# Kernel optimization log

Hardware: AMD Instinct MI355X
Metric: run time of the kernel (lower is better)

## Reference

```python
import jax, jax.numpy as jnp
import numpy as np

N_NODES = 100_000
N_EDGES = 3_200_000  # avg in-degree 32
N_CLASSES = 16
TEMP = 0.5


def setup_inputs() -> dict:
    key = jax.random.key(0)
    k1, k2, k3 = jax.random.split(key, 3)
    src = jax.random.randint(k1, (N_EDGES,), 0, N_NODES, dtype=jnp.int32)
    # guarantee every node has at least one incoming edge so scatter-mean
    # and the sharpening normalization are well-defined
    dst = jnp.concatenate([
        jnp.arange(N_NODES, dtype=jnp.int32),
        jax.random.randint(k2, (N_EDGES - N_NODES,), 0, N_NODES, dtype=jnp.int32),
    ])
    edge_index = jnp.stack([src, dst], axis=0)  # [2, E]
    # positive predictions (log is taken downstream)
    aug_pred = jax.random.uniform(k3, (N_NODES, N_CLASSES), jnp.float32, 1e-3, 1.0)
    return {"edge_index": edge_index, "aug_pred": aug_pred}


def reference(edge_index, aug_pred):
    src = edge_index[0]  # message source nodes
    dst = edge_index[1]  # aggregation targets
    E = edge_index.shape[1]

    # scatter-mean aggregation: avg_pred[i] = mean_{e: dst[e]=i} aug_pred[src[e]]
    msg = aug_pred[src]                                   # [E, C]
    sums = jax.ops.segment_sum(msg, dst, num_segments=N_NODES)
    cnt = jax.ops.segment_sum(jnp.ones((E,), aug_pred.dtype), dst,
                              num_segments=N_NODES)
    avg_pred = sums / jnp.maximum(cnt, 1.0)[:, None]      # [N, C]

    # temperature sharpening + normalize
    p = avg_pred ** (1.0 / TEMP)
    sharp_avg_pred = p / jnp.sum(p, axis=1, keepdims=True)

    # edge-indexed gathers; dst side is detached in the original
    s = (avg_pred + 1e-10)[src]                            # [E, C]
    d = jax.lax.stop_gradient(sharp_avg_pred + 1e-10)[dst]  # [E, C]

    cr_loss = (d * jnp.log(d) - d * jnp.log(s)).sum(axis=1)  # [E]
    return cr_loss.mean()
```

## Files before the change

kernel.cpp:

```cpp
#include <hip/hip_runtime.h>

#define NCLS 16
#define NB 391
#define BSH 8
#define TILE 4096
#define KPT 16
#define PREB 512
#define BMAX 9216
#define ACAP 9

static __device__ __forceinline__ float bflo(unsigned u) {
  return __uint_as_float(u << 16);
}
static __device__ __forceinline__ float bfhi(unsigned u) {
  return __uint_as_float(u & 0xFFFF0000u);
}
static __device__ __forceinline__ unsigned f2bf1(float f) {
  unsigned u = __float_as_uint(f);
  return (u + 0x7FFF + ((u >> 16) & 1)) >> 16;
}
static __device__ __forceinline__ unsigned packbf(float a, float b) {
  return f2bf1(a) | (f2bf1(b) << 16);
}

__global__ void pre_kernel(const int* __restrict__ dstv, int* __restrict__ bcnt, int E,
                           const float2* __restrict__ aug, unsigned* __restrict__ augh, int n2) {
  __shared__ int lh[NB];
  if (blockIdx.x < PREB) {
    for (int t = threadIdx.x; t < NB; t += 256) lh[t] = 0;
    __syncthreads();
    int stride = PREB * 256;
    for (int i = blockIdx.x * 256 + threadIdx.x; i < E; i += stride)
      atomicAdd(&lh[dstv[i] >> BSH], 1);
    __syncthreads();
    for (int t = threadIdx.x; t < NB; t += 256) {
      int v = lh[t];
      if (v) atomicAdd(&bcnt[t], v);
    }
  } else {
    int i = (blockIdx.x - PREB) * 256 + threadIdx.x;
    if (i < n2) {
      float2 v = aug[i];
      augh[i] = packbf(v.x, v.y);
    }
  }
}

__global__ void bscan_kernel(const int* __restrict__ bcnt, int* __restrict__ bbase,
                             int* __restrict__ gcur) {
  __shared__ int tmp[512];
  int t = threadIdx.x;
  int x = (t < NB) ? bcnt[t] : 0;
  tmp[t] = x;
  __syncthreads();
  for (int o = 1; o < 512; o <<= 1) {
    int v = (t >= o) ? tmp[t - o] : 0;
    __syncthreads();
    tmp[t] += v;
    __syncthreads();
  }
  if (t < NB) { int e = tmp[t] - x; bbase[t] = e; gcur[t] = e; }
  if (t == NB - 1) bbase[NB] = tmp[t];
}

__global__ void __launch_bounds__(256) bin_kernel(const int* __restrict__ srcv,
                                                  const int* __restrict__ dstv,
                                                  int* __restrict__ gcur,
                                                  int* __restrict__ packed, int E) {
  __shared__ int hist[NB];
  __shared__ int off[NB];
  __shared__ int delta[NB];
  __shared__ int part[16];
  __shared__ int2 stag[TILE];
  int tid = threadIdx.x;
  int base = blockIdx.x * TILE;
  int cnt = min(TILE, E - base);
  for (int t = tid; t < NB; t += 256) hist[t] = 0;
  __syncthreads();
  int myw[KPT];
  int myp[KPT];
#pragma unroll
  for (int k = 0; k < KPT; k++) {
    int idx = tid + k * 256;
    myw[k] = -1;
    myp[k] = 0;
    if (idx < cnt) {
      int s = srcv[base + idx], d = dstv[base + idx];
      int b = d >> BSH;
      int r = atomicAdd(&hist[b], 1);
      myw[k] = s | ((d & 255) << 17);
      myp[k] = (b << 12) | r;
    }
  }
  __syncthreads();
  if (tid < 16) {
    int s = 0;
    int lo = tid * 25, hiX = min(NB, lo + 25);
    for (int j = lo; j < hiX; j++) { int v = hist[j]; off[j] = s; s += v; }
    part[tid] = s;
  }
  __syncthreads();
  if (tid == 0) {
    int run = 0;
    for (int j = 0; j < 16; j++) { int v = part[j]; part[j] = run; run += v; }
  }
  __syncthreads();
  for (int t = tid; t < NB; t += 256) off[t] += part[t / 25];
  __syncthreads();
  for (int t = tid; t < NB; t += 256) {
    int c = hist[t];
    int gb = c ? atomicAdd(&gcur[t], c) : 0;
    delta[t] = gb - off[t];
  }
  __syncthreads();
#pragma unroll
  for (int k = 0; k < KPT; k++) {
    if (myw[k] >= 0) {
      int b = myp[k] >> 12, r = myp[k] & 4095;
      int p = off[b] + r;
      int2 w;
      w.x = myw[k];
      w.y = p + delta[b];
      stag[p] = w;
    }
  }
  __syncthreads();
  for (int i = tid; i < cnt; i += 256) {
    int2 w = stag[i];
    packed[w.y] = w.x;
  }
}

__global__ void __launch_bounds__(1024) agg_kernel(const int* __restrict__ bbase,
                                                   const int* __restrict__ packed,
                                                   const unsigned* __restrict__ augh,
                                                   unsigned* __restrict__ logs,
                                                   float* __restrict__ dvec,
                                                   double* __restrict__ acc, int N) {
  __shared__ int ssrc[BMAX];
  __shared__ int hist[256];
  __shared__ int off[256];
  __shared__ float red[16];
  int tid = threadIdx.x;
  int b = blockIdx.x;
  int rbeg = bbase[b], rend = bbase[b + 1];
  if (tid < 256) hist[tid] = 0;
  __syncthreads();
  int myw[ACAP];
  int myr[ACAP];
#pragma unroll
  for (int k = 0; k < ACAP; k++) {
    int i = rbeg + tid + k * 1024;
    int w = (i < rend) ? packed[i] : -1;
    myw[k] = w;
    myr[k] = (w >= 0) ? atomicAdd(&hist[w >> 17], 1) : 0;
  }
  __syncthreads();
  if (tid < 64) {
    int h0 = hist[4 * tid], h1 = hist[4 * tid + 1];
    int h2 = hist[4 * tid + 2], h3 = hist[4 * tid + 3];
    int tot = h0 + h1 + h2 + h3;
    int inc = tot;
#pragma unroll
    for (int o = 1; o < 64; o <<= 1) {
      int u = __shfl_up(inc, o, 64);
      if (tid >= o) inc += u;
    }
    int exc = inc - tot;
    off[4 * tid] = exc;
    off[4 * tid + 1] = exc + h0;
    off[4 * tid + 2] = exc + h0 + h1;
    off[4 * tid + 3] = exc + h0 + h1 + h2;
  }
  __syncthreads();
#pragma unroll
  for (int k = 0; k < ACAP; k++) {
    int w = myw[k];
    if (w >= 0) ssrc[off[w >> 17] + myr[k]] = w & 0x1FFFF;
  }
  __syncthreads();
  int node = tid >> 2, lane = tid & 3;
  int boff = off[node];
  int deg = hist[node];
  double s0 = 0., s1 = 0., s2 = 0., s3 = 0.;
  int wsh = lane << 1;
  int e = 0;
  for (; e + 8 <= deg; e += 8) {
    int q0 = ssrc[boff + e],     q1 = ssrc[boff + e + 1];
    int q2 = ssrc[boff + e + 2], q3 = ssrc[boff + e + 3];
    int q4 = ssrc[boff + e + 4], q5 = ssrc[boff + e + 5];
    int q6 = ssrc[boff + e + 6], q7 = ssrc[boff + e + 7];
    uint2 g0 = *reinterpret_cast<const uint2*>(augh + ((size_t)q0 << 3) + wsh);
    uint2 g1 = *reinterpret_cast<const uint2*>(augh + ((size_t)q1 << 3) + wsh);
    uint2 g2 = *reinterpret_cast<const uint2*>(augh + ((size_t)q2 << 3) + wsh);
    uint2 g3 = *reinterpret_cast<const uint2*>(augh + ((size_t)q3 << 3) + wsh);
    uint2 g4 = *reinterpret_cast<const uint2*>(augh + ((size_t)q4 << 3) + wsh);
    uint2 g5 = *reinterpret_cast<const uint2*>(augh + ((size_t)q5 << 3) + wsh);
    uint2 g6 = *reinterpret_cast<const uint2*>(augh + ((size_t)q6 << 3) + wsh);
    uint2 g7 = *reinterpret_cast<const uint2*>(augh + ((size_t)q7 << 3) + wsh);
    s0 += (double)bflo(g0.x) + (double)bflo(g1.x) + (double)bflo(g2.x) + (double)bflo(g3.x) +
          (double)bflo(g4.x) + (double)bflo(g5.x) + (double)bflo(g6.x) + (double)bflo(g7.x);
    s1 += (double)bfhi(g0.x) + (double)bfhi(g1.x) + (double)bfhi(g2.x) + (double)bfhi(g3.x) +
          (double)bfhi(g4.x) + (double)bfhi(g5.x) + (double)bfhi(g6.x) + (double)bfhi(g7.x);
    s2 += (double)bflo(g0.y) + (double)bflo(g1.y) + (double)bflo(g2.y) + (double)bflo(g3.y) +
          (double)bflo(g4.y) + (double)bflo(g5.y) + (double)bflo(g6.y) + (double)bflo(g7.y);
    s3 += (double)bfhi(g0.y) + (double)bfhi(g1.y) + (double)bfhi(g2.y) + (double)bfhi(g3.y) +
          (double)bfhi(g4.y) + (double)bfhi(g5.y) + (double)bfhi(g6.y) + (double)bfhi(g7.y);
  }
  for (; e < deg; e++) {
    int q0 = ssrc[boff + e];
    uint2 g0 = *reinterpret_cast<const uint2*>(augh + ((size_t)q0 << 3) + wsh);
    s0 += (double)bflo(g0.x); s1 += (double)bfhi(g0.x);
    s2 += (double)bflo(g0.y); s3 += (double)bfhi(g0.y);
  }
  double dinv = 1.0 / (double)(deg > 0 ? deg : 1);
  float a0 = (float)(s0 * dinv), a1 = (float)(s1 * dinv);
  float a2 = (float)(s2 * dinv), a3 = (float)(s3 * dinv);
  float p2 = a0 * a0 + a1 * a1 + a2 * a2 + a3 * a3;
  p2 += __shfl_xor(p2, 1, 64);
  p2 += __shfl_xor(p2, 2, 64);
  float ip = 1.0f / p2;
  float d0 = a0 * a0 * ip + 1e-10f, d1 = a1 * a1 * ip + 1e-10f;
  float d2 = a2 * a2 * ip + 1e-10f, d3 = a3 * a3 * ip + 1e-10f;
  float h = d0 * __logf(d0) + d1 * __logf(d1) + d2 * __logf(d2) + d3 * __logf(d3);
  h += __shfl_xor(h, 1, 64);
  h += __shfl_xor(h, 2, 64);
  int g = (b << BSH) + node;
  float contrib = 0.f;
  if (g < N) {
    uint2 lw;
    lw.x = packbf(__logf(a0 + 1e-10f), __logf(a1 + 1e-10f));
    lw.y = packbf(__logf(a2 + 1e-10f), __logf(a3 + 1e-10f));
    *reinterpret_cast<uint2*>(logs + ((size_t)g << 3) + wsh) = lw;
    float4 dd;
    dd.x = d0; dd.y = d1; dd.z = d2; dd.w = d3;
    *reinterpret_cast<float4*>(dvec + ((size_t)g << 4) + (lane << 2)) = dd;
    if (lane == 0) contrib = (float)deg * h;
  }
#pragma unroll
  for (int o = 32; o >= 1; o >>= 1) contrib += __shfl_xor(contrib, o, 64);
  if ((tid & 63) == 0) red[tid >> 6] = contrib;
  __syncthreads();
  if (tid == 0) {
    float s = 0.f;
#pragma unroll
    for (int wv = 0; wv < 16; wv++) s += red[wv];
    atomicAdd(acc, (double)s);
  }
}

#define ASTR 17
__global__ void __launch_bounds__(1024) loss_kernel(const int* __restrict__ bbase,
                                                    const int* __restrict__ packed,
                                                    const unsigned* __restrict__ logs,
                                                    const float* __restrict__ dvec,
                                                    double* __restrict__ acc, int N) {
  __shared__ float sdv[256 * ASTR];
  __shared__ double red[16];
  int tid = threadIdx.x;
  int b = blockIdx.x;
  int rbeg = bbase[b], rend = bbase[b + 1];
  int nb0 = b << BSH;
  {
    const float4* gsrc = reinterpret_cast<const float4*>(dvec + ((size_t)nb0 << 4));
    int nvalid = min(256, N - nb0);
    int nf4 = nvalid * 4;
    for (int i = tid; i < nf4; i += 1024) {
      float4 v = gsrc[i];
      float* r = sdv + (i >> 2) * ASTR + ((i & 3) << 2);
      r[0] = v.x; r[1] = v.y; r[2] = v.z; r[3] = v.w;
    }
  }
  __syncthreads();
  double dot = 0.0;
  int i = rbeg + tid;
  for (; i + 1024 < rend; i += 2048) {
    int wa = packed[i];
    int wb = packed[i + 1024];
    int sa = wa & 0x1FFFF, la = wa >> 17;
    int sb = wb & 0x1FFFF, lb = wb >> 17;
    const uint4* ga = reinterpret_cast<const uint4*>(logs + ((size_t)sa << 3));
    const uint4* gb = reinterpret_cast<const uint4*>(logs + ((size_t)sb << 3));
    uint4 a0 = ga[0], a1 = ga[1];
    uint4 b0 = gb[0], b1 = gb[1];
    const float* ra = sdv + la * ASTR;
    const float* rb = sdv + lb * ASTR;
    float ea = ra[0] * bflo(a0.x) + ra[1] * bfhi(a0.x) +
               ra[2] * bflo(a0.y) + ra[3] * bfhi(a0.y) +
               ra[4] * bflo(a0.z) + ra[5] * bfhi(a0.z) +
               ra[6] * bflo(a0.w) + ra[7] * bfhi(a0.w) +
               ra[8] * bflo(a1.x) + ra[9] * bfhi(a1.x) +
               ra[10] * bflo(a1.y) + ra[11] * bfhi(a1.y) +
               ra[12] * bflo(a1.z) + ra[13] * bfhi(a1.z) +
               ra[14] * bflo(a1.w) + ra[15] * bfhi(a1.w);
    float eb = rb[0] * bflo(b0.x) + rb[1] * bfhi(b0.x) +
               rb[2] * bflo(b0.y) + rb[3] * bfhi(b0.y) +
               rb[4] * bflo(b0.z) + rb[5] * bfhi(b0.z) +
               rb[6] * bflo(b0.w) + rb[7] * bfhi(b0.w) +
               rb[8] * bflo(b1.x) + rb[9] * bfhi(b1.x) +
               rb[10] * bflo(b1.y) + rb[11] * bfhi(b1.y) +
               rb[12] * bflo(b1.z) + rb[13] * bfhi(b1.z) +
               rb[14] * bflo(b1.w) + rb[15] * bfhi(b1.w);
    dot += (double)ea + (double)eb;
  }
  if (i < rend) {
    int wa = packed[i];
    int sa = wa & 0x1FFFF, la = wa >> 17;
    const uint4* ga = reinterpret_cast<const uint4*>(logs + ((size_t)sa << 3));
    uint4 a0 = ga[0], a1 = ga[1];
    const float* ra = sdv + la * ASTR;
    float ea = ra[0] * bflo(a0.x) + ra[1] * bfhi(a0.x) +
               ra[2] * bflo(a0.y) + ra[3] * bfhi(a0.y) +
               ra[4] * bflo(a0.z) + ra[5] * bfhi(a0.z) +
               ra[6] * bflo(a0.w) + ra[7] * bfhi(a0.w) +
               ra[8] * bflo(a1.x) + ra[9] * bfhi(a1.x) +
               ra[10] * bflo(a1.y) + ra[11] * bfhi(a1.y) +
               ra[12] * bflo(a1.z) + ra[13] * bfhi(a1.z) +
               ra[14] * bflo(a1.w) + ra[15] * bfhi(a1.w);
    dot += (double)ea;
  }
#pragma unroll
  for (int o = 32; o >= 1; o >>= 1) dot += __shfl_xor(dot, o, 64);
  if ((tid & 63) == 0) red[tid >> 6] = dot;
  __syncthreads();
  if (tid == 0) {
    double s = 0.0;
#pragma unroll
    for (int wv = 0; wv < 16; wv++) s += red[wv];
    atomicAdd(acc, -s);
  }
}

__global__ void finalize_kernel(const double* __restrict__ acc,
                                float* __restrict__ out, int E) {
  if (threadIdx.x == 0 && blockIdx.x == 0)
    out[0] = (float)(acc[0] / (double)E);
}

extern "C" void kernel_launch(void* const* d_in, const int* in_sizes, int n_in,
                              void* d_out, int out_size, void* d_ws, size_t ws_size,
                              hipStream_t stream) {
  const int* edge_index = (const int*)d_in[0];
  const float* aug_pred = (const float*)d_in[1];
  const int E = in_sizes[0] / 2;
  const int N = in_sizes[1] / NCLS;

  const int* srcv = edge_index;
  const int* dstv = edge_index + E;

  char* p = (char*)d_ws;
  auto alloc = [&](size_t bytes) {
    char* r = p;
    p += (bytes + 255) & ~(size_t)255;
    return r;
  };
  double* acc = (double*)alloc(8);
  int* bcnt = (int*)alloc(NB * 4);
  int* bbase = (int*)alloc((NB + 1) * 4);
  int* gcur = (int*)alloc(NB * 4);
  int* packed = (int*)alloc((size_t)E * 4);
  unsigned* augh = (unsigned*)alloc((size_t)N * NCLS * 2);
  unsigned* logs = (unsigned*)alloc((size_t)N * NCLS * 2);
  float* dvec = (float*)alloc((size_t)N * NCLS * 4);

  size_t zero_bytes = (size_t)((char*)bbase - (char*)d_ws);
  hipMemsetAsync(d_ws, 0, zero_bytes, stream);

  int n2 = N * NCLS / 2;
  int cvtb = (n2 + 255) / 256;
  pre_kernel<<<PREB + cvtb, 256, 0, stream>>>(dstv, bcnt, E, (const float2*)aug_pred, augh, n2);
  bscan_kernel<<<1, 512, 0, stream>>>(bcnt, bbase, gcur);
  int tiles = (E + TILE - 1) / TILE;
  bin_kernel<<<tiles, 256, 0, stream>>>(srcv, dstv, gcur, packed, E);
  agg_kernel<<<NB, 1024, 0, stream>>>(bbase, packed, augh, logs, dvec, acc, N);
  loss_kernel<<<NB, 1024, 0, stream>>>(bbase, packed, logs, dvec, acc, N);
  finalize_kernel<<<1, 64, 0, stream>>>(acc, (float*)d_out, E);
}
```

Measured before the change: 176.5 us.

## Write CSR-sorted edges in agg and factor loss into per-node gathered log sums

The aggregation kernel now writes its shared-memory per-node sorted source list back to global memory along with a per-node CSR offsets array. The loss kernel then gives each destination node four lanes that sum the gathered bf16 log rows of its sources and dot that sum once with the node's d vector. This replaces the per-edge 16-wide dot product and the shared-memory d staging. It adds an extra global write of the edge list in agg, and lanes may be unevenly loaded because node degrees differ.

```diff
diff --git a/kernel.cpp b/kernel.cpp
--- a/kernel.cpp
+++ b/kernel.cpp
@@ -47,7 +47,8 @@
 }
 
 __global__ void bscan_kernel(const int* __restrict__ bcnt, int* __restrict__ bbase,
-                             int* __restrict__ gcur) {
+                             int* __restrict__ gcur, int* __restrict__ offsets,
+                             int N, int E) {
   __shared__ int tmp[512];
   int t = threadIdx.x;
   int x = (t < NB) ? bcnt[t] : 0;
@@ -61,6 +62,7 @@
   }
   if (t < NB) { int e = tmp[t] - x; bbase[t] = e; gcur[t] = e; }
   if (t == NB - 1) bbase[NB] = tmp[t];
+  if (t == 0) offsets[N] = E;
 }
 
 __global__ void __launch_bounds__(256) bin_kernel(const int* __restrict__ srcv,
@@ -132,10 +134,11 @@
 }
 
 __global__ void __launch_bounds__(1024) agg_kernel(const int* __restrict__ bbase,
-                                                   const int* __restrict__ packed,
+                                                   int* __restrict__ packed,
                                                    const unsigned* __restrict__ augh,
                                                    unsigned* __restrict__ logs,
                                                    float* __restrict__ dvec,
+                                                   int* __restrict__ offsets,
                                                    double* __restrict__ acc, int N) {
   __shared__ int ssrc[BMAX];
   __shared__ int hist[256];
@@ -179,6 +182,12 @@
     if (w >= 0) ssrc[off[w >> 17] + myr[k]] = w & 0x1FFFF;
   }
   __syncthreads();
+  {
+    int bcount = rend - rbeg;
+    for (int i = tid; i < bcount; i += 1024) packed[rbeg + i] = ssrc[i];
+    int g2 = (b << BSH) + tid;
+    if (tid < 256 && g2 < N) offsets[g2] = rbeg + off[tid];
+  }
   int node = tid >> 2, lane = tid & 3;
   int boff = off[node];
   int deg = hist[node];
@@ -249,75 +258,53 @@
   }
 }
 
-#define ASTR 17
-__global__ void __launch_bounds__(1024) loss_kernel(const int* __restrict__ bbase,
+__global__ void __launch_bounds__(1024) loss_kernel(const int* __restrict__ offsets,
                                                     const int* __restrict__ packed,
                                                     const unsigned* __restrict__ logs,
                                                     const float* __restrict__ dvec,
                                                     double* __restrict__ acc, int N) {
-  __shared__ float sdv[256 * ASTR];
   __shared__ double red[16];
   int tid = threadIdx.x;
   int b = blockIdx.x;
-  int rbeg = bbase[b], rend = bbase[b + 1];
-  int nb0 = b << BSH;
-  {
-    const float4* gsrc = reinterpret_cast<const float4*>(dvec + ((size_t)nb0 << 4));
-    int nvalid = min(256, N - nb0);
-    int nf4 = nvalid * 4;
-    for (int i = tid; i < nf4; i += 1024) {
-      float4 v = gsrc[i];
-      float* r = sdv + (i >> 2) * ASTR + ((i & 3) << 2);
-      r[0] = v.x; r[1] = v.y; r[2] = v.z; r[3] = v.w;
-    }
-  }
-  __syncthreads();
+  int node = tid >> 2, lane = tid & 3;
+  int g = (b << BSH) + node;
   double dot = 0.0;
-  int i = rbeg + tid;
-  for (; i + 1024 < rend; i += 2048) {
-    int wa = packed[i];
-    int wb = packed[i + 1024];
-    int sa = wa & 0x1FFFF, la = wa >> 17;
-    int sb = wb & 0x1FFFF, lb = wb >> 17;
-    const uint4* ga = reinterpret_cast<const uint4*>(logs + ((size_t)sa << 3));
-    const uint4* gb = reinterpret_cast<const uint4*>(logs + ((size_t)sb << 3));
-    uint4 a0 = ga[0], a1 = ga[1];
-    uint4 b0 = gb[0], b1 = gb[1];
-    const float* ra = sdv + la * ASTR;
-    const float* rb = sdv + lb * ASTR;
-    float ea = ra[0] * bflo(a0.x) + ra[1] * bfhi(a0.x) +
-               ra[2] * bflo(a0.y) + ra[3] * bfhi(a0.y) +
-               ra[4] * bflo(a0.z) + ra[5] * bfhi(a0.z) +
-               ra[6] * bflo(a0.w) + ra[7] * bfhi(a0.w) +
-               ra[8] * bflo(a1.x) + ra[9] * bfhi(a1.x) +
-               ra[10] * bflo(a1.y) + ra[11] * bfhi(a1.y) +
-               ra[12] * bflo(a1.z) + ra[13] * bfhi(a1.z) +
-               ra[14] * bflo(a1.w) + ra[15] * bfhi(a1.w);
-    float eb = rb[0] * bflo(b0.x) + rb[1] * bfhi(b0.x) +
-               rb[2] * bflo(b0.y) + rb[3] * bfhi(b0.y) +
-               rb[4] * bflo(b0.z) + rb[5] * bfhi(b0.z) +
-               rb[6] * bflo(b0.w) + rb[7] * bfhi(b0.w) +
-               rb[8] * bflo(b1.x) + rb[9] * bfhi(b1.x) +
-               rb[10] * bflo(b1.y) + rb[11] * bfhi(b1.y) +
-               rb[12] * bflo(b1.z) + rb[13] * bfhi(b1.z) +
-               rb[14] * bflo(b1.w) + rb[15] * bfhi(b1.w);
-    dot += (double)ea + (double)eb;
-  }
-  if (i < rend) {
-    int wa = packed[i];
-    int sa = wa & 0x1FFFF, la = wa >> 17;
-    const uint4* ga = reinterpret_cast<const uint4*>(logs + ((size_t)sa << 3));
-    uint4 a0 = ga[0], a1 = ga[1];
-    const float* ra = sdv + la * ASTR;
-    float ea = ra[0] * bflo(a0.x) + ra[1] * bfhi(a0.x) +
-               ra[2] * bflo(a0.y) + ra[3] * bfhi(a0.y) +
-               ra[4] * bflo(a0.z) + ra[5] * bfhi(a0.z) +
-               ra[6] * bflo(a0.w) + ra[7] * bfhi(a0.w) +
-               ra[8] * bflo(a1.x) + ra[9] * bfhi(a1.x) +
-               ra[10] * bflo(a1.y) + ra[11] * bfhi(a1.y) +
-               ra[12] * bflo(a1.z) + ra[13] * bfhi(a1.z) +
-               ra[14] * bflo(a1.w) + ra[15] * bfhi(a1.w);
-    dot += (double)ea;
+  if (g < N) {
+    int beg = offsets[g], end = offsets[g + 1];
+    int deg = end - beg;
+    double s0 = 0., s1 = 0., s2 = 0., s3 = 0.;
+    int wsh = lane << 1;
+    int e = 0;
+    for (; e + 8 <= deg; e += 8) {
+      int q0 = packed[beg + e],     q1 = packed[beg + e + 1];
+      int q2 = packed[beg + e + 2], q3 = packed[beg + e + 3];
+      int q4 = packed[beg + e + 4], q5 = packed[beg + e + 5];
+      int q6 = packed[beg + e + 6], q7 = packed[beg + e + 7];
+      uint2 g0 = *reinterpret_cast<const uint2*>(logs + ((size_t)q0 << 3) + wsh);
+      uint2 g1 = *reinterpret_cast<const uint2*>(logs + ((size_t)q1 << 3) + wsh);
+      uint2 g2 = *reinterpret_cast<const uint2*>(logs + ((size_t)q2 << 3) + wsh);
+      uint2 g3 = *reinterpret_cast<const uint2*>(logs + ((size_t)q3 << 3) + wsh);
+      uint2 g4 = *reinterpret_cast<const uint2*>(logs + ((size_t)q4 << 3) + wsh);
+      uint2 g5 = *reinterpret_cast<const uint2*>(logs + ((size_t)q5 << 3) + wsh);
+      uint2 g6 = *reinterpret_cast<const uint2*>(logs + ((size_t)q6 << 3) + wsh);
+      uint2 g7 = *reinterpret_cast<const uint2*>(logs + ((size_t)q7 << 3) + wsh);
+      s0 += (double)bflo(g0.x) + (double)bflo(g1.x) + (double)bflo(g2.x) + (double)bflo(g3.x) +
+            (double)bflo(g4.x) + (double)bflo(g5.x) + (double)bflo(g6.x) + (double)bflo(g7.x);
+      s1 += (double)bfhi(g0.x) + (double)bfhi(g1.x) + (double)bfhi(g2.x) + (double)bfhi(g3.x) +
+            (double)bfhi(g4.x) + (double)bfhi(g5.x) + (double)bfhi(g6.x) + (double)bfhi(g7.x);
+      s2 += (double)bflo(g0.y) + (double)bflo(g1.y) + (double)bflo(g2.y) + (double)bflo(g3.y) +
+            (double)bflo(g4.y) + (double)bflo(g5.y) + (double)bflo(g6.y) + (double)bflo(g7.y);
+      s3 += (double)bfhi(g0.y) + (double)bfhi(g1.y) + (double)bfhi(g2.y) + (double)bfhi(g3.y) +
+            (double)bfhi(g4.y) + (double)bfhi(g5.y) + (double)bfhi(g6.y) + (double)bfhi(g7.y);
+    }
+    for (; e < deg; e++) {
+      int q0 = packed[beg + e];
+      uint2 g0 = *reinterpret_cast<const uint2*>(logs + ((size_t)q0 << 3) + wsh);
+      s0 += (double)bflo(g0.x); s1 += (double)bfhi(g0.x);
+      s2 += (double)bflo(g0.y); s3 += (double)bfhi(g0.y);
+    }
+    float4 dd = *reinterpret_cast<const float4*>(dvec + ((size_t)g << 4) + (lane << 2));
+    dot = (double)dd.x * s0 + (double)dd.y * s1 + (double)dd.z * s2 + (double)dd.w * s3;
   }
 #pragma unroll
   for (int o = 32; o >= 1; o >>= 1) dot += __shfl_xor(dot, o, 64);
@@ -359,6 +346,7 @@
   int* bbase = (int*)alloc((NB + 1) * 4);
   int* gcur = (int*)alloc(NB * 4);
   int* packed = (int*)alloc((size_t)E * 4);
+  int* offsets = (int*)alloc((size_t)(N + 1) * 4);
   unsigned* augh = (unsigned*)alloc((size_t)N * NCLS * 2);
   unsigned* logs = (unsigned*)alloc((size_t)N * NCLS * 2);
   float* dvec = (float*)alloc((size_t)N * NCLS * 4);
@@ -369,10 +357,10 @@
   int n2 = N * NCLS / 2;
   int cvtb = (n2 + 255) / 256;
   pre_kernel<<<PREB + cvtb, 256, 0, stream>>>(dstv, bcnt, E, (const float2*)aug_pred, augh, n2);
-  bscan_kernel<<<1, 512, 0, stream>>>(bcnt, bbase, gcur);
+  bscan_kernel<<<1, 512, 0, stream>>>(bcnt, bbase, gcur, offsets, N, E);
   int tiles = (E + TILE - 1) / TILE;
   bin_kernel<<<tiles, 256, 0, stream>>>(srcv, dstv, gcur, packed, E);
-  agg_kernel<<<NB, 1024, 0, stream>>>(bbase, packed, augh, logs, dvec, acc, N);
-  loss_kernel<<<NB, 1024, 0, stream>>>(bbase, packed, logs, dvec, acc, N);
+  agg_kernel<<<NB, 1024, 0, stream>>>(bbase, packed, augh, logs, dvec, offsets, acc, N);
+  loss_kernel<<<NB, 1024, 0, stream>>>(offsets, packed, logs, dvec, acc, N);
   finalize_kernel<<<1, 64, 0, stream>>>(acc, (float*)d_out, E);
 }
```

New measurement: 190.3 us. 1.08x slower.
